# Kernel tuning notes

Measured on AMD Instinct MI355X. Metric: run time of the kernel, lower is better.

The kernel has to match this reference:

```python
import jax, jax.numpy as jnp
import numpy as np
from jax import lax

SEQ, BS, D_IN, D_H, D_OUT, N_LAYERS = 784, 256, 1, 512, 1, 3

def _glorot(key, shape):
    fan_in, fan_out = shape[0], shape[1]
    std = jnp.sqrt(2.0 / (fan_in + fan_out))
    return (jax.random.normal(key, shape) * std).astype(jnp.float32)

def setup_inputs() -> dict:
    key = jax.random.key(0)
    ks = jax.random.split(key, 3 + 3 * N_LAYERS + 2)
    x = jax.random.normal(ks[0], (SEQ, BS, D_IN), dtype=jnp.float32)
    W0 = _glorot(ks[1], (D_IN, D_H))
    b0 = jnp.zeros((D_H,), jnp.float32)
    # per-layer recurrence params, stacked: a (L,D_H), B (L,D_H,D_H), C (L,D_H,D_H)
    a = jnp.stack([jax.random.uniform(ks[2 + i], (D_H,), minval=0.999, maxval=1.001) for i in range(N_LAYERS)]).astype(jnp.float32)
    B = jnp.stack([_glorot(ks[2 + N_LAYERS + i], (D_H, D_H)) for i in range(N_LAYERS)])
    C = jnp.stack([_glorot(ks[2 + 2 * N_LAYERS + i], (D_H, D_H)) for i in range(N_LAYERS)])
    Wf = _glorot(ks[2 + 3 * N_LAYERS], (D_H, D_OUT))
    bf = jnp.zeros((D_OUT,), jnp.float32)
    return {"x": x, "W0": W0, "b0": b0, "a": a, "B": B, "C": C, "Wf": Wf, "bf": bf}

def _rnn_layer(x, a_l, B_l, C_l):
    # x: (seq, bs, d_h); diagonal linear recurrence h_t = h_{t-1} * a + x_t @ B
    xb = jnp.einsum('sbi,ih->sbh', x, B_l)  # precompute input projection
    def step(h, xt):
        h = h * a_l + xt
        return h, h
    _, hs = lax.scan(step, jnp.zeros((x.shape[1], a_l.shape[0]), x.dtype), xb)
    return jnp.einsum('sbh,ho->sbo', hs, C_l)

def reference(x, W0, b0, a, B, C, Wf, bf):
    identity = x  # use_downsampling=False, use_residual=True
    h = jax.nn.relu(x @ W0 + b0)
    for l in range(N_LAYERS):
        h = jax.nn.relu(_rnn_layer(h, a[l], B[l], C[l]))
    out = h @ Wf + bf
    return out + identity
```

## Files before the change

kernel.cpp:

```cpp
#include <hip/hip_runtime.h>
#include <hip/hip_bf16.h>

#define SEQ 784
#define BS  256
#define DH  512
#define MT  (SEQ * BS)
#define NL  3
#define NC  14
#define CL  56
#define COLS (BS * DH)

typedef unsigned short u16;
typedef __bf16  bf16x8  __attribute__((ext_vector_type(8)));
typedef float   f32x4   __attribute__((ext_vector_type(4)));
typedef unsigned short ushort8 __attribute__((ext_vector_type(8)));

__device__ __forceinline__ u16 f2b(float f) {
    unsigned int x = __float_as_uint(f);
    unsigned int r = (x + 0x7FFFu + ((x >> 16) & 1u)) >> 16;
    return (u16)r;
}
__device__ __forceinline__ float b2f(u16 u) {
    return __uint_as_float(((unsigned int)u) << 16);
}

__global__ __launch_bounds__(256) void prep_k(const float* __restrict__ B,
                                              const float* __restrict__ C,
                                              u16* __restrict__ Bp,
                                              u16* __restrict__ Cp)
{
    const long t = (long)blockIdx.x * 256 + threadIdx.x;
    const int  e  = (int)(t & 7);
    const int  l  = (int)((t >> 3) & 63);
    const int  ni = (int)((t >> 9) & 3);
    const int  wd = (int)((t >> 11) & 7);
    const int  g  = (int)((t >> 14) & 15);
    const long lay = t >> 18;
    const int  n = wd * 64 + ni * 16 + (l & 15);
    const int  k = g * 32 + (l >> 4) * 8 + e;
    const long src = (lay << 18) + (long)k * DH + n;
    Bp[t] = f2b(B[src]);
    Cp[t] = f2b(C[src]);
}

__global__ __launch_bounds__(256) void h0_k(const float* __restrict__ x,
                                            const float* __restrict__ W0,
                                            const float* __restrict__ b0,
                                            u16* __restrict__ out)
{
    const long t  = (long)blockIdx.x * 256 + threadIdx.x;
    const long m  = t >> 6;
    const int  j0 = (int)(t & 63) * 8;
    const float xv = x[m];
    ushort8 o;
#pragma unroll
    for (int j = 0; j < 8; ++j)
        o[j] = f2b(fmaxf(fmaf(xv, W0[j0 + j], b0[j0 + j]), 0.f));
    *(ushort8*)&out[m * DH + j0] = o;
}

template <int RELU>
__global__ __launch_bounds__(512, 4) void gemm_ip(const u16* __restrict__ X,
                                                  const u16* __restrict__ Wp,
                                                  u16* __restrict__ Y)
{
    __shared__ __align__(16) u16 lds[64 * 512];

    const int tid  = threadIdx.x;
    const int lane = tid & 63;
    const int wid  = tid >> 6;
    const long bm  = (long)blockIdx.x * 64;

    const int srow = tid >> 3;
    const int scol = (((tid & 7) ^ (srow & 7)) * 8);
    const u16* gax = X + (bm + srow) * DH + scol;

    f32x4 acc[4][4];
#pragma unroll
    for (int i = 0; i < 4; ++i)
#pragma unroll
        for (int j = 0; j < 4; ++j)
            acc[i][j] = (f32x4){0.f, 0.f, 0.f, 0.f};

    __builtin_amdgcn_global_load_lds(
        (const __attribute__((address_space(1))) void*)gax,
        (__attribute__((address_space(3))) void*)
            ((__attribute__((address_space(3))) char*)lds + tid * 16),
        16, 0, 0);

    for (int t = 0; t < 8; ++t) {
        __syncthreads();
        if (t < 7) {
            __builtin_amdgcn_global_load_lds(
                (const __attribute__((address_space(1))) void*)(gax + (t + 1) * 64),
                (__attribute__((address_space(3))) void*)
                    ((__attribute__((address_space(3))) char*)lds +
                     ((t + 1) & 1) * 8192 + tid * 16),
                16, 0, 0);
        }
        const u16* Atile = lds + (t & 1) * 4096;

#pragma unroll
        for (int kk = 0; kk < 2; ++kk) {
            bf16x8 bv[4];
#pragma unroll
            for (int ni = 0; ni < 4; ++ni)
                bv[ni] = *(const bf16x8*)&Wp[((long)((2 * t + kk) * 32 + wid * 4 + ni) << 9)
                                             + (lane << 3)];
            const int fcol = ((kk * 4 + (lane >> 4)) ^ (lane & 7)) * 8;
            bf16x8 af[4];
#pragma unroll
            for (int i = 0; i < 4; ++i)
                af[i] = *(const bf16x8*)&Atile[(i * 16 + (lane & 15)) * 64 + fcol];
#pragma unroll
            for (int mi = 0; mi < 4; ++mi)
#pragma unroll
                for (int ni = 0; ni < 4; ++ni)
                    acc[mi][ni] = __builtin_amdgcn_mfma_f32_16x16x32_bf16(
                        af[mi], bv[ni], acc[mi][ni], 0, 0, 0);
        }
    }
    __syncthreads();

    u16* Ctile = lds;
    const int rbase = (lane >> 4) * 4;
    const int cloc  = wid * 64 + (lane & 15);
#pragma unroll
    for (int mi = 0; mi < 4; ++mi)
#pragma unroll
        for (int ni = 0; ni < 4; ++ni)
#pragma unroll
            for (int r = 0; r < 4; ++r) {
                float v = acc[mi][ni][r];
                if (RELU) v = fmaxf(v, 0.f);
                const int row = mi * 16 + rbase + r;
                const int col = (cloc + ni * 16) ^ (((row >> 2) & 3) * 16);
                Ctile[row * 512 + col] = f2b(v);
            }
    __syncthreads();
#pragma unroll
    for (int p = 0; p < 8; ++p) {
        const int e   = p * 4096 + tid * 8;
        const int row = e >> 9;
        const int col = e & 511;
        const int csw = col ^ (((row >> 2) & 3) * 16);
        *(ushort8*)&Y[(bm + row) * DH + col] = *(const ushort8*)&Ctile[row * 512 + csw];
    }
}

__global__ __launch_bounds__(256) void scanA_k(const u16* __restrict__ buf,
                                               const float* __restrict__ a_all,
                                               int layer,
                                               float* __restrict__ carry)
{
    const long T  = (long)blockIdx.x * 256 + threadIdx.x;
    const int col = (int)(T & (COLS - 1));
    const int c   = (int)(T >> 17);
    const float av = a_all[layer * DH + (col & (DH - 1))];
    const u16* p = buf + (long)c * CL * COLS + col;

    float h = 0.f;
    float pre[8];
#pragma unroll
    for (int i = 0; i < 8; ++i) pre[i] = b2f(p[(long)i * COLS]);
    for (int s8 = 0; s8 < CL; s8 += 8) {
        const bool more = (s8 + 8) < CL;
#pragma unroll
        for (int j = 0; j < 8; ++j) {
            const float v = pre[j];
            if (more) pre[j] = b2f(p[(long)(s8 + 8 + j) * COLS]);
            h = fmaf(h, av, v);
        }
    }
    carry[T] = h;
}

__global__ __launch_bounds__(256) void scanB_k(float* __restrict__ carry,
                                               const float* __restrict__ a_all,
                                               int layer)
{
    const int col = blockIdx.x * 256 + threadIdx.x;
    const float av = a_all[layer * DH + (col & (DH - 1))];
    float a2 = av * av, a4 = a2 * a2, a8 = a4 * a4;
    float a16 = a8 * a8, a32 = a16 * a16;
    const float pw = a32 * a16 * a8;

    float cin = 0.f;
    for (int c = 0; c < NC; ++c) {
        float cr = carry[(long)c * COLS + col];
        carry[(long)c * COLS + col] = cin;
        cin = fmaf(cin, pw, cr);
    }
}

__global__ __launch_bounds__(256) void scanC_k(u16* __restrict__ buf,
                                               const float* __restrict__ a_all,
                                               int layer,
                                               const float* __restrict__ carry)
{
    const long T  = (long)blockIdx.x * 256 + threadIdx.x;
    const int col = (int)(T & (COLS - 1));
    const int c   = (int)(T >> 17);
    const float av = a_all[layer * DH + (col & (DH - 1))];
    u16* p = buf + (long)c * CL * COLS + col;

    float h = carry[T];
    float pre[8];
#pragma unroll
    for (int i = 0; i < 8; ++i) pre[i] = b2f(p[(long)i * COLS]);
    for (int s8 = 0; s8 < CL; s8 += 8) {
        const bool more = (s8 + 8) < CL;
#pragma unroll
        for (int j = 0; j < 8; ++j) {
            const float v = pre[j];
            if (more) pre[j] = b2f(p[(long)(s8 + 8 + j) * COLS]);
            h = fmaf(h, av, v);
            p[(long)(s8 + j) * COLS] = f2b(h);
        }
    }
}

__global__ __launch_bounds__(256) void final_k(const u16* __restrict__ h,
                                               const float* __restrict__ Wf,
                                               const float* __restrict__ bf_,
                                               const float* __restrict__ x,
                                               float* __restrict__ out)
{
    const long m  = (long)blockIdx.x * 4 + (threadIdx.x >> 6);
    const int lane = threadIdx.x & 63;
    const ushort8 v = *(const ushort8*)&h[m * DH + lane * 8];
    float s = 0.f;
#pragma unroll
    for (int j = 0; j < 8; ++j) s += b2f(v[j]) * Wf[lane * 8 + j];
#pragma unroll
    for (int off = 32; off > 0; off >>= 1) s += __shfl_down(s, off, 64);
    if (lane == 0) out[m] = s + bf_[0] + x[m];
}

extern "C" void kernel_launch(void* const* d_in, const int* in_sizes, int n_in,
                              void* d_out, int out_size, void* d_ws, size_t ws_size,
                              hipStream_t stream)
{
    const float* x   = (const float*)d_in[0];
    const float* W0  = (const float*)d_in[1];
    const float* b0  = (const float*)d_in[2];
    const float* a   = (const float*)d_in[3];
    const float* B   = (const float*)d_in[4];
    const float* C   = (const float*)d_in[5];
    const float* Wf  = (const float*)d_in[6];
    const float* bf_ = (const float*)d_in[7];
    float* out = (float*)d_out;

    const long BUF = (long)MT * DH;
    const size_t need = (size_t)BUF * 2 + 2ULL * 3 * DH * DH * 2
                      + (size_t)NC * COLS * 4;
    if (ws_size < need) return;

    u16*   buf   = (u16*)d_ws;
    u16*   Bp    = buf + BUF;
    u16*   Cp    = Bp + 3L * DH * DH;
    float* carry = (float*)(Cp + 3L * DH * DH);

    prep_k<<<(3 * DH * DH) / 256, 256, 0, stream>>>(B, C, Bp, Cp);
    h0_k<<<(MT * 64) / 256, 256, 0, stream>>>(x, W0, b0, buf);

    for (int l = 0; l < NL; ++l) {
        gemm_ip<0><<<MT / 64, 512, 0, stream>>>(buf, Bp + (long)l * DH * DH, buf);
        scanA_k<<<(NC * COLS) / 256, 256, 0, stream>>>(buf, a, l, carry);
        scanB_k<<<COLS / 256, 256, 0, stream>>>(carry, a, l);
        scanC_k<<<(NC * COLS) / 256, 256, 0, stream>>>(buf, a, l, carry);
        gemm_ip<1><<<MT / 64, 512, 0, stream>>>(buf, Cp + (long)l * DH * DH, buf);
    }
    final_k<<<MT / 4, 256, 0, stream>>>(buf, Wf, bf_, x, out);
}
```

Before: 1.017 ms.

## Fuse input projection into first GEMM and output head into last GEMM

```diff
diff --git a/kernel.cpp b/kernel.cpp
--- a/kernel.cpp
+++ b/kernel.cpp
@@ -43,21 +43,6 @@
     Cp[t] = f2b(C[src]);
 }
 
-__global__ __launch_bounds__(256) void h0_k(const float* __restrict__ x,
-                                            const float* __restrict__ W0,
-                                            const float* __restrict__ b0,
-                                            u16* __restrict__ out)
-{
-    const long t  = (long)blockIdx.x * 256 + threadIdx.x;
-    const long m  = t >> 6;
-    const int  j0 = (int)(t & 63) * 8;
-    const float xv = x[m];
-    ushort8 o;
-#pragma unroll
-    for (int j = 0; j < 8; ++j)
-        o[j] = f2b(fmaxf(fmaf(xv, W0[j0 + j], b0[j0 + j]), 0.f));
-    *(ushort8*)&out[m * DH + j0] = o;
-}
 
 template <int RELU>
 __global__ __launch_bounds__(512, 4) void gemm_ip(const u16* __restrict__ X,
@@ -148,6 +133,198 @@
     }
 }
 
+__global__ __launch_bounds__(512, 4) void gemm_first(const float* __restrict__ x,
+                                                     const float* __restrict__ W0,
+                                                     const float* __restrict__ b0,
+                                                     const u16* __restrict__ Wp,
+                                                     u16* __restrict__ Y)
+{
+    __shared__ __align__(16) u16 lds[64 * 512];
+
+    const int tid  = threadIdx.x;
+    const int lane = tid & 63;
+    const int wid  = tid >> 6;
+    const long bm  = (long)blockIdx.x * 64;
+
+    const int prow = tid >> 3;
+    const int slot = tid & 7;
+    const float xv = x[bm + prow];
+
+#pragma unroll
+    for (int t = 0; t < 8; ++t) {
+        const int k0 = t * 64 + ((slot ^ (prow & 7)) * 8);
+        ushort8 o;
+#pragma unroll
+        for (int e = 0; e < 8; ++e)
+            o[e] = f2b(fmaxf(fmaf(xv, W0[k0 + e], b0[k0 + e]), 0.f));
+        *(ushort8*)&lds[t * 4096 + tid * 8] = o;
+    }
+
+    f32x4 acc[4][4];
+#pragma unroll
+    for (int i = 0; i < 4; ++i)
+#pragma unroll
+        for (int j = 0; j < 4; ++j)
+            acc[i][j] = (f32x4){0.f, 0.f, 0.f, 0.f};
+
+    __syncthreads();
+
+#pragma unroll
+    for (int t = 0; t < 8; ++t) {
+        const u16* Atile = lds + t * 4096;
+#pragma unroll
+        for (int kk = 0; kk < 2; ++kk) {
+            bf16x8 bv[4];
+#pragma unroll
+            for (int ni = 0; ni < 4; ++ni)
+                bv[ni] = *(const bf16x8*)&Wp[((long)((2 * t + kk) * 32 + wid * 4 + ni) << 9)
+                                             + (lane << 3)];
+            const int fcol = ((kk * 4 + (lane >> 4)) ^ (lane & 7)) * 8;
+            bf16x8 af[4];
+#pragma unroll
+            for (int i = 0; i < 4; ++i)
+                af[i] = *(const bf16x8*)&Atile[(i * 16 + (lane & 15)) * 64 + fcol];
+#pragma unroll
+            for (int mi = 0; mi < 4; ++mi)
+#pragma unroll
+                for (int ni = 0; ni < 4; ++ni)
+                    acc[mi][ni] = __builtin_amdgcn_mfma_f32_16x16x32_bf16(
+                        af[mi], bv[ni], acc[mi][ni], 0, 0, 0);
+        }
+    }
+    __syncthreads();
+
+    u16* Ctile = lds;
+    const int rbase = (lane >> 4) * 4;
+    const int cloc  = wid * 64 + (lane & 15);
+#pragma unroll
+    for (int mi = 0; mi < 4; ++mi)
+#pragma unroll
+        for (int ni = 0; ni < 4; ++ni)
+#pragma unroll
+            for (int r = 0; r < 4; ++r) {
+                const int row = mi * 16 + rbase + r;
+                const int col = (cloc + ni * 16) ^ (((row >> 2) & 3) * 16);
+                Ctile[row * 512 + col] = f2b(acc[mi][ni][r]);
+            }
+    __syncthreads();
+#pragma unroll
+    for (int p = 0; p < 8; ++p) {
+        const int e   = p * 4096 + tid * 8;
+        const int row = e >> 9;
+        const int col = e & 511;
+        const int csw = col ^ (((row >> 2) & 3) * 16);
+        *(ushort8*)&Y[(bm + row) * DH + col] = *(const ushort8*)&Ctile[row * 512 + csw];
+    }
+}
+
+__global__ __launch_bounds__(512, 4) void gemm_last(const u16* __restrict__ X,
+                                                    const u16* __restrict__ Wp,
+                                                    const float* __restrict__ Wf,
+                                                    const float* __restrict__ bf_,
+                                                    const float* __restrict__ x,
+                                                    float* __restrict__ out)
+{
+    __shared__ __align__(16) u16 lds[64 * 512];
+    float* partials = (float*)lds;
+
+    const int tid  = threadIdx.x;
+    const int lane = tid & 63;
+    const int wid  = tid >> 6;
+    const long bm  = (long)blockIdx.x * 64;
+
+    const int srow = tid >> 3;
+    const int scol = (((tid & 7) ^ (srow & 7)) * 8);
+    const u16* gax = X + (bm + srow) * DH + scol;
+
+    f32x4 acc[4][4];
+#pragma unroll
+    for (int i = 0; i < 4; ++i)
+#pragma unroll
+        for (int j = 0; j < 4; ++j)
+            acc[i][j] = (f32x4){0.f, 0.f, 0.f, 0.f};
+
+    __builtin_amdgcn_global_load_lds(
+        (const __attribute__((address_space(1))) void*)gax,
+        (__attribute__((address_space(3))) void*)
+            ((__attribute__((address_space(3))) char*)lds + tid * 16),
+        16, 0, 0);
+
+    for (int t = 0; t < 8; ++t) {
+        __syncthreads();
+        if (t < 7) {
+            __builtin_amdgcn_global_load_lds(
+                (const __attribute__((address_space(1))) void*)(gax + (t + 1) * 64),
+                (__attribute__((address_space(3))) void*)
+                    ((__attribute__((address_space(3))) char*)lds +
+                     ((t + 1) & 1) * 8192 + tid * 16),
+                16, 0, 0);
+        }
+        const u16* Atile = lds + (t & 1) * 4096;
+
+#pragma unroll
+        for (int kk = 0; kk < 2; ++kk) {
+            bf16x8 bv[4];
+#pragma unroll
+            for (int ni = 0; ni < 4; ++ni)
+                bv[ni] = *(const bf16x8*)&Wp[((long)((2 * t + kk) * 32 + wid * 4 + ni) << 9)
+                                             + (lane << 3)];
+            const int fcol = ((kk * 4 + (lane >> 4)) ^ (lane & 7)) * 8;
+            bf16x8 af[4];
+#pragma unroll
+            for (int i = 0; i < 4; ++i)
+                af[i] = *(const bf16x8*)&Atile[(i * 16 + (lane & 15)) * 64 + fcol];
+#pragma unroll
+            for (int mi = 0; mi < 4; ++mi)
+#pragma unroll
+                for (int ni = 0; ni < 4; ++ni)
+                    acc[mi][ni] = __builtin_amdgcn_mfma_f32_16x16x32_bf16(
+                        af[mi], bv[ni], acc[mi][ni], 0, 0, 0);
+        }
+    }
+    __syncthreads();
+
+    const int cbase = wid * 64 + (lane & 15);
+    float wf[4];
+#pragma unroll
+    for (int ni = 0; ni < 4; ++ni) wf[ni] = Wf[cbase + ni * 16];
+
+    float part[4][4];
+#pragma unroll
+    for (int mi = 0; mi < 4; ++mi)
+#pragma unroll
+        for (int r = 0; r < 4; ++r) {
+            float s = 0.f;
+#pragma unroll
+            for (int ni = 0; ni < 4; ++ni)
+                s = fmaf(fmaxf(acc[mi][ni][r], 0.f), wf[ni], s);
+            part[mi][r] = s;
+        }
+#pragma unroll
+    for (int mi = 0; mi < 4; ++mi)
+#pragma unroll
+        for (int r = 0; r < 4; ++r) {
+#pragma unroll
+            for (int off = 1; off < 16; off <<= 1)
+                part[mi][r] += __shfl_xor(part[mi][r], off, 64);
+        }
+    if ((lane & 15) == 0) {
+        const int q = lane >> 4;
+#pragma unroll
+        for (int mi = 0; mi < 4; ++mi)
+#pragma unroll
+            for (int r = 0; r < 4; ++r)
+                partials[wid * 64 + mi * 16 + q * 4 + r] = part[mi][r];
+    }
+    __syncthreads();
+    if (tid < 64) {
+        float s = 0.f;
+#pragma unroll
+        for (int w = 0; w < 8; ++w) s += partials[w * 64 + tid];
+        out[bm + tid] = s + bf_[0] + x[bm + tid];
+    }
+}
+
 __global__ __launch_bounds__(256) void scanA_k(const u16* __restrict__ buf,
                                                const float* __restrict__ a_all,
                                                int layer,
@@ -218,23 +395,6 @@
             p[(long)(s8 + j) * COLS] = f2b(h);
         }
     }
-}
-
-__global__ __launch_bounds__(256) void final_k(const u16* __restrict__ h,
-                                               const float* __restrict__ Wf,
-                                               const float* __restrict__ bf_,
-                                               const float* __restrict__ x,
-                                               float* __restrict__ out)
-{
-    const long m  = (long)blockIdx.x * 4 + (threadIdx.x >> 6);
-    const int lane = threadIdx.x & 63;
-    const ushort8 v = *(const ushort8*)&h[m * DH + lane * 8];
-    float s = 0.f;
-#pragma unroll
-    for (int j = 0; j < 8; ++j) s += b2f(v[j]) * Wf[lane * 8 + j];
-#pragma unroll
-    for (int off = 32; off > 0; off >>= 1) s += __shfl_down(s, off, 64);
-    if (lane == 0) out[m] = s + bf_[0] + x[m];
 }
 
 extern "C" void kernel_launch(void* const* d_in, const int* in_sizes, int n_in,
@@ -262,14 +422,21 @@
     float* carry = (float*)(Cp + 3L * DH * DH);
 
     prep_k<<<(3 * DH * DH) / 256, 256, 0, stream>>>(B, C, Bp, Cp);
-    h0_k<<<(MT * 64) / 256, 256, 0, stream>>>(x, W0, b0, buf);
 
     for (int l = 0; l < NL; ++l) {
-        gemm_ip<0><<<MT / 64, 512, 0, stream>>>(buf, Bp + (long)l * DH * DH, buf);
+        if (l == 0)
+            gemm_first<<<MT / 64, 512, 0, stream>>>(x, W0, b0, Bp, buf);
+        else
+            gemm_ip<0><<<MT / 64, 512, 0, stream>>>(buf, Bp + (long)l * DH * DH, buf);
+
         scanA_k<<<(NC * COLS) / 256, 256, 0, stream>>>(buf, a, l, carry);
         scanB_k<<<COLS / 256, 256, 0, stream>>>(carry, a, l);
         scanC_k<<<(NC * COLS) / 256, 256, 0, stream>>>(buf, a, l, carry);
-        gemm_ip<1><<<MT / 64, 512, 0, stream>>>(buf, Cp + (long)l * DH * DH, buf);
-    }
-    final_k<<<MT / 4, 256, 0, stream>>>(buf, Wf, bf_, x, out);
-}
+
+        if (l == NL - 1)
+            gemm_last<<<MT / 64, 512, 0, stream>>>(buf, Cp + (long)l * DH * DH,
+                                                   Wf, bf_, x, out);
+        else
+            gemm_ip<1><<<MT / 64, 512, 0, stream>>>(buf, Cp + (long)l * DH * DH, buf);
+    }
+}
```

Measured after the change: 940.7 us. 1.08x faster.
